# Kernel optimization log

Measured on AMD Instinct MI355X. Metric: run time of the kernel, lower is better.

The kernel has to match this reference:

```python
import jax, jax.numpy as jnp
import numpy as np

WS = 7
SHIFT = 3
NH = 16
DIM = 512
MLP = 2048
EMB = 512
EPS = 1e-6


def _rel_pos_index(ws):
    coords = np.stack(np.meshgrid(np.arange(ws), np.arange(ws), indexing='ij'))  # [2,ws,ws]
    flat = coords.reshape(2, -1)
    rel = flat[:, :, None] - flat[:, None, :]          # [2,N,N]
    rel = rel.transpose(1, 2, 0).copy()                # [N,N,2]
    rel[..., 0] += ws - 1
    rel[..., 1] += ws - 1
    rel[..., 0] *= 2 * ws - 1
    return rel.sum(-1)                                 # [N,N] int


def _shift_mask(H, W, ws, shift):
    img = np.zeros((H, W))
    cnt = 0
    for hs in (slice(0, -ws), slice(-ws, -shift), slice(-shift, None)):
        for wsl in (slice(0, -ws), slice(-ws, -shift), slice(-shift, None)):
            img[hs, wsl] = cnt
            cnt += 1
    win = img.reshape(H // ws, ws, W // ws, ws).transpose(0, 2, 1, 3).reshape(-1, ws * ws)
    diff = win[:, None, :] - win[:, :, None]           # [nW,N,N]
    return np.where(diff != 0, -100.0, 0.0).astype(np.float32)


def setup_inputs() -> dict:
    key = jax.random.key(0)
    ks = jax.random.split(key, 16)
    B, H, W = 16, 56, 56
    C, mlp, emb_dim = DIM, MLP, EMB
    std = 0.02
    inp = {
        'x': jax.random.normal(ks[0], (B, H * W, C), jnp.float32),
        'emb': jax.random.normal(ks[1], (B, emb_dim), jnp.float32),
        'adaLN_w': jax.random.normal(ks[2], (emb_dim, 6 * C), jnp.float32) * std,
        'adaLN_b': jnp.zeros((6 * C,), jnp.float32),
        'qkv_w': jax.random.normal(ks[3], (C, 3 * C), jnp.float32) * std,
        'qkv_b': jnp.zeros((3 * C,), jnp.float32),
        'proj_w': jax.random.normal(ks[4], (C, C), jnp.float32) * std,
        'proj_b': jnp.zeros((C,), jnp.float32),
        'rel_bias_table': jax.random.normal(ks[5], ((2 * WS - 1) ** 2, NH), jnp.float32) * std,
        'ff_w1': jax.random.normal(ks[6], (C, mlp), jnp.float32) * std,
        'ff_b1': jnp.zeros((mlp,), jnp.float32),
        'ff_w2': jax.random.normal(ks[7], (mlp, C), jnp.float32) * std,
        'ff_b2': jnp.zeros((C,), jnp.float32),
        'H': H,
        'W': W,
    }
    return inp


def _ln(t):
    mu = t.mean(-1, keepdims=True)
    var = ((t - mu) ** 2).mean(-1, keepdims=True)
    return (t - mu) / jnp.sqrt(var + EPS)


def reference(x, emb, adaLN_w, adaLN_b, qkv_w, qkv_b, proj_w, proj_b,
              rel_bias_table, ff_w1, ff_b1, ff_w2, ff_b2, H, W):
    B, L, C = x.shape
    dh = C // NH
    scale = dh ** (-0.5)
    N = WS * WS
    nWh, nWw = H // WS, W // WS
    nW = nWh * nWw

    # AdaLN modulation
    mod = jax.nn.silu(emb) @ adaLN_w + adaLN_b
    sh_sa, sc_sa, g_sa, sh_ff, sc_ff, g_ff = jnp.split(mod, 6, axis=-1)

    h = _ln(x) * (1.0 + sc_sa[:, None, :]) + sh_sa[:, None, :]
    h = h.reshape(B, H, W, C)
    h = jnp.roll(h, (-SHIFT, -SHIFT), axis=(1, 2))

    # window partition -> [B*nW, N, C]
    win = h.reshape(B, nWh, WS, nWw, WS, C).transpose(0, 1, 3, 2, 4, 5).reshape(B * nW, N, C)

    qkv = (win @ qkv_w + qkv_b).reshape(B * nW, N, 3, NH, dh).transpose(2, 0, 3, 1, 4)
    q, k, v = qkv[0], qkv[1], qkv[2]                   # [B_, NH, N, dh]
    attn = jnp.einsum('bhnd,bhmd->bhnm', q, k) * scale

    idx = _rel_pos_index(WS)
    bias = rel_bias_table[idx.reshape(-1)].reshape(N, N, NH).transpose(2, 0, 1)
    attn = attn + bias[None]

    mask = jnp.asarray(_shift_mask(H, W, WS, SHIFT))   # [nW,N,N]
    attn = attn.reshape(B, nW, NH, N, N) + mask[None, :, None]
    attn = jax.nn.softmax(attn.reshape(B * nW, NH, N, N), axis=-1)

    out = jnp.einsum('bhnm,bhmd->bnhd', attn, v).reshape(B * nW, N, C)
    out = out @ proj_w + proj_b

    # window reverse + unshift
    h = out.reshape(B, nWh, nWw, WS, WS, C).transpose(0, 1, 3, 2, 4, 5).reshape(B, H, W, C)
    h = jnp.roll(h, (SHIFT, SHIFT), axis=(1, 2)).reshape(B, L, C)

    x = x + g_sa[:, None, :] * h

    h = _ln(x) * (1.0 + sc_ff[:, None, :]) + sh_ff[:, None, :]
    ffo = jax.nn.gelu(h @ ff_w1 + ff_b1, approximate=False) @ ff_w2 + ff_b2
    return x + g_ff[:, None, :] * ffo
```

## Files before the change

kernel.cpp:

```cpp
#include <hip/hip_runtime.h>
#include <cmath>

typedef unsigned short u16;
typedef unsigned short u16x2 __attribute__((ext_vector_type(2)));
typedef unsigned short u16x4 __attribute__((ext_vector_type(4)));
typedef unsigned short u16x8 __attribute__((ext_vector_type(8)));
typedef short s16x8 __attribute__((ext_vector_type(8)));
typedef float f32x4 __attribute__((ext_vector_type(4)));
typedef float f32x2 __attribute__((ext_vector_type(2)));

#define B_SZ 16
#define HW 56
#define L_TOK 3136
#define C_DIM 512
#define NHEAD 16
#define DHEAD 32
#define WS7 7
#define NWIN 49
#define ROWS_TOTAL 50176
#define MLP_DIM 2048

__device__ __forceinline__ float bf2f(u16 u) {
    union { unsigned int i; float f; } z;
    z.i = ((unsigned int)u) << 16;
    return z.f;
}
__device__ __forceinline__ u16 f2bf(float f) {
    union { float f; unsigned int i; } z;
    z.f = f;
    unsigned int r = z.i + 0x7fffu + ((z.i >> 16) & 1u);
    return (u16)(r >> 16);
}

__device__ __forceinline__ void gl_lds16(const u16* g, u16* l) {
    __builtin_amdgcn_global_load_lds(
        (const __attribute__((address_space(1))) unsigned int*)g,
        (__attribute__((address_space(3))) unsigned int*)l,
        16, 0, 0);
}

__global__ __launch_bounds__(256)
void mod_kernel(const float* __restrict__ emb, const float* __restrict__ w,
                const float* __restrict__ bias, float* __restrict__ mod)
{
    int b = blockIdx.y;
    int o = blockIdx.x * 256 + threadIdx.x;
    __shared__ float se[512];
    for (int i = threadIdx.x; i < 512; i += 256) {
        float e = emb[b * 512 + i];
        se[i] = e / (1.0f + expf(-e));
    }
    __syncthreads();
    float acc = bias[o];
    #pragma unroll 8
    for (int k = 0; k < 512; ++k)
        acc += se[k] * w[(size_t)k * 3072 + o];
    mod[b * 3072 + o] = acc;
}

__global__ __launch_bounds__(1024)
void transpose_kernel(const float* __restrict__ W, u16* __restrict__ Wt, int K, int N)
{
    __shared__ float tile[32][33];
    int k0 = blockIdx.x * 32, n0 = blockIdx.y * 32;
    tile[threadIdx.y][threadIdx.x] = W[(size_t)(k0 + threadIdx.y) * N + (n0 + threadIdx.x)];
    __syncthreads();
    Wt[(size_t)(n0 + threadIdx.y) * K + (k0 + threadIdx.x)] = f2bf(tile[threadIdx.x][threadIdx.y]);
}

template<int WINDOWED>
__global__ __launch_bounds__(256)
void ln_kernel(const float* __restrict__ xin, const float* __restrict__ mod,
               u16* __restrict__ out, int shOff, int scOff, int rowBase)
{
    int wv   = threadIdx.x >> 6;
    int lane = threadIdx.x & 63;
    int rbl = blockIdx.x * 4 + wv;
    int rb  = rbl + rowBase;
    int b = rb / L_TOK, l = rb - b * L_TOK;
    const float* xr = xin + (size_t)rb * C_DIM;
    int c0 = lane * 8;
    f32x4 u0 = *(const f32x4*)(xr + c0);
    f32x4 u1 = *(const f32x4*)(xr + c0 + 4);
    float s = u0.x + u0.y + u0.z + u0.w + u1.x + u1.y + u1.z + u1.w;
    float q = u0.x*u0.x + u0.y*u0.y + u0.z*u0.z + u0.w*u0.w
            + u1.x*u1.x + u1.y*u1.y + u1.z*u1.z + u1.w*u1.w;
    #pragma unroll
    for (int off = 32; off > 0; off >>= 1) {
        s += __shfl_xor(s, off);
        q += __shfl_xor(q, off);
    }
    float mu = s * (1.0f / 512.0f);
    float var = q * (1.0f / 512.0f) - mu * mu;
    float rstd = rsqrtf(var + 1e-6f);
    const float* mb = mod + b * 3072;
    f32x4 sc0 = *(const f32x4*)(mb + scOff + c0);
    f32x4 sc1 = *(const f32x4*)(mb + scOff + c0 + 4);
    f32x4 sh0 = *(const f32x4*)(mb + shOff + c0);
    f32x4 sh1 = *(const f32x4*)(mb + shOff + c0 + 4);
    float y[8];
    y[0] = (u0.x - mu) * rstd * (1.0f + sc0.x) + sh0.x;
    y[1] = (u0.y - mu) * rstd * (1.0f + sc0.y) + sh0.y;
    y[2] = (u0.z - mu) * rstd * (1.0f + sc0.z) + sh0.z;
    y[3] = (u0.w - mu) * rstd * (1.0f + sc0.w) + sh0.w;
    y[4] = (u1.x - mu) * rstd * (1.0f + sc1.x) + sh1.x;
    y[5] = (u1.y - mu) * rstd * (1.0f + sc1.y) + sh1.y;
    y[6] = (u1.z - mu) * rstd * (1.0f + sc1.z) + sh1.z;
    y[7] = (u1.w - mu) * rstd * (1.0f + sc1.w) + sh1.w;
    size_t drow;
    if (WINDOWED) {
        int hh = l / HW, ww = l - hh * HW;
        int hs = hh - 3; if (hs < 0) hs += HW;
        int ws2 = ww - 3; if (ws2 < 0) ws2 += HW;
        int wi = (hs / WS7) * 8 + (ws2 / WS7);
        int n  = (hs % WS7) * WS7 + (ws2 % WS7);
        int b_local = rbl / L_TOK;
        drow = (size_t)((b_local * 64 + wi) * NWIN + n);
    } else {
        drow = (size_t)rbl;
    }
    u16x8 o;
    #pragma unroll
    for (int i = 0; i < 8; ++i) o[i] = f2bf(y[i]);
    *(u16x8*)(out + drow * C_DIM + c0) = o;
}

template<int EPI>
__global__ __launch_bounds__(256)
void gemm128(const u16* __restrict__ A, const u16* __restrict__ Bt,
             const float* __restrict__ bias, void* __restrict__ outv,
             const float* __restrict__ resid, const float* __restrict__ mod,
             int N, int K, int rowOffset)
{
    __shared__ u16 sA[3][128][32];
    __shared__ u16 sB[3][128][32];
    const int tid  = threadIdx.x;
    const int lane = tid & 63;
    const int wave = tid >> 6;
    const int wr = (wave >> 1) * 64;
    const int wc = (wave & 1) * 64;
    const int quad = lane >> 4;
    const int mrow = lane & 15;
    const int rowBase = blockIdx.x * 128;
    const int colBase = blockIdx.y * 128;

    const int r0   = wave * 32;
    const int lrow = lane >> 2;
    const int lcol = (lane & 3) * 8;
    const u16* gA = A  + (size_t)(rowBase + r0 + lrow) * K + lcol;
    const u16* gB = Bt + (size_t)(colBase + r0 + lrow) * K + lcol;
    const size_t gstep = (size_t)16 * K;

    f32x4 acc[4][4] = {};
    const int nt = K >> 5;

#define STAGE(bi, kk) do {                                 \
    gl_lds16(gA + (kk),         &sA[bi][r0][0]);           \
    gl_lds16(gA + (kk) + gstep, &sA[bi][r0 + 16][0]);      \
    gl_lds16(gB + (kk),         &sB[bi][r0][0]);           \
    gl_lds16(gB + (kk) + gstep, &sB[bi][r0 + 16][0]);      \
} while (0)

    STAGE(0, 0);
    STAGE(1, 32);
    asm volatile("s_waitcnt vmcnt(4)" ::: "memory");
    __builtin_amdgcn_s_barrier();

    int cur = 0, pre = 2;
    for (int t = 0; t < nt; ++t) {
        if (t + 2 < nt) STAGE(pre, (t + 2) * 32);
        s16x8 af[4], bg[4];
        #pragma unroll
        for (int tt = 0; tt < 4; ++tt) {
            af[tt] = *(const s16x8*)&sA[cur][wr + tt * 16 + mrow][quad * 8];
            bg[tt] = *(const s16x8*)&sB[cur][wc + tt * 16 + mrow][quad * 8];
        }
        #pragma unroll
        for (int tm = 0; tm < 4; ++tm)
            #pragma unroll
            for (int tn = 0; tn < 4; ++tn)
                acc[tm][tn] = __builtin_amdgcn_mfma_f32_16x16x32_bf16(
                    af[tm], bg[tn], acc[tm][tn], 0, 0, 0);
        if (t + 1 < nt) {
            if (t + 2 < nt)
                asm volatile("s_waitcnt vmcnt(4) lgkmcnt(0)" ::: "memory");
            else
                asm volatile("s_waitcnt vmcnt(0) lgkmcnt(0)" ::: "memory");
            __builtin_amdgcn_s_barrier();
        }
        cur = (cur == 2) ? 0 : cur + 1;
        pre = (pre == 2) ? 0 : pre + 1;
    }
#undef STAGE

    #pragma unroll
    for (int tm = 0; tm < 4; ++tm) {
        #pragma unroll
        for (int tn = 0; tn < 4; ++tn) {
            int col = colBase + wc + tn * 16 + mrow;
            float bv = bias[col];
            #pragma unroll
            for (int i = 0; i < 4; ++i) {
                int r = rowBase + wr + tm * 16 + quad * 4 + i;
                float v = acc[tm][tn][i] + bv;
                if constexpr (EPI == 0) {
                    ((u16*)outv)[(size_t)r * N + col] = f2bf(v);
                } else if constexpr (EPI == 1) {
                    float g = 0.5f * v * (1.0f + erff(v * 0.70710678118654752f));
                    ((u16*)outv)[(size_t)r * N + col] = f2bf(g);
                } else if constexpr (EPI == 2) {
                    int rg = r + rowOffset;
                    int b = rg / L_TOK;
                    int rem = rg - b * L_TOK;
                    int wi = rem / NWIN;
                    int n  = rem - wi * NWIN;
                    int hs  = (wi >> 3) * WS7 + n / WS7;
                    int ws2 = (wi & 7) * WS7 + n % WS7;
                    int hh = hs + 3;  if (hh >= HW)  hh -= HW;
                    int ww = ws2 + 3; if (ww >= HW)  ww -= HW;
                    size_t dst = ((size_t)(b * L_TOK + hh * HW + ww)) * C_DIM + col;
                    float g = mod[b * 3072 + 1024 + col];
                    ((float*)outv)[dst] = resid[dst] + g * v;
                } else {
                    int rg = r + rowOffset;
                    int b = rg / L_TOK;
                    size_t dst = (size_t)rg * C_DIM + col;
                    float g = mod[b * 3072 + 2560 + col];
                    ((float*)outv)[dst] = resid[dst] + g * v;
                }
            }
        }
    }
}

__global__ __launch_bounds__(256)
void attn_mfma(const u16* __restrict__ qkv, const float* __restrict__ bias_table,
               u16* __restrict__ out)
{
    const int w    = blockIdx.x;
    const int hg   = blockIdx.y;
    const int wave = threadIdx.x >> 6;
    const int lane = threadIdx.x & 63;
    const int h    = hg * 4 + wave;
    const int wi   = w & 63;
    const int quad = lane >> 4;
    const int mrow = lane & 15;

    __shared__ u16 sP[4][64][72];
    __shared__ u16 sVt[4][32][72];
    __shared__ float sBias[4][169];

    const u16* qb = qkv + (size_t)w * NWIN * 1536 + h * DHEAD;

    for (int e = lane; e < 169; e += 64)
        sBias[wave][e] = bias_table[e * NHEAD + h];

    #pragma unroll
    for (int rr = 0; rr < 4; ++rr) {
        int e = rr * 64 + lane;
        int r = e >> 2, d0 = (e & 3) * 8;
        u16x8 vv = {};
        if (e < 196)
            vv = *(const u16x8*)(qb + (size_t)r * 1536 + 1024 + d0);
        #pragma unroll
        for (int j = 0; j < 8; ++j)
            sVt[wave][d0 + j][r] = vv[j];
    }

    s16x8 qf[4], kf[4];
    #pragma unroll
    for (int t = 0; t < 4; ++t) {
        int r = t * 16 + mrow; if (r > 48) r = 48;
        qf[t] = *(const s16x8*)(qb + (size_t)r * 1536 + quad * 8);
        kf[t] = *(const s16x8*)(qb + (size_t)r * 1536 + 512 + quad * 8);
    }
    __syncthreads();

    f32x4 sacc[4][4] = {};
    #pragma unroll
    for (int tm = 0; tm < 4; ++tm)
        #pragma unroll
        for (int tn = 0; tn < 4; ++tn)
            sacc[tm][tn] = __builtin_amdgcn_mfma_f32_16x16x32_bf16(
                qf[tm], kf[tn], sacc[tm][tn], 0, 0, 0);

    const float scale = 0.17677669529663687f;
    const int wh = wi >> 3, ww = wi & 7;

    int khA[4], kwA[4], rkA[4], nOK[4];
    #pragma unroll
    for (int tn = 0; tn < 4; ++tn) {
        int n = tn * 16 + mrow;
        nOK[tn] = (n < NWIN);
        int nc = n > 48 ? 48 : n;
        khA[tn] = nc / 7; kwA[tn] = nc - khA[tn] * 7;
        int gkh = wh * 7 + khA[tn], gkw = ww * 7 + kwA[tn];
        rkA[tn] = (gkh < 49 ? 0 : (gkh < 53 ? 1 : 2)) * 3
                + (gkw < 49 ? 0 : (gkw < 53 ? 1 : 2));
    }

    #pragma unroll
    for (int tm = 0; tm < 4; ++tm) {
        #pragma unroll
        for (int i = 0; i < 4; ++i) {
            int m = tm * 16 + quad * 4 + i;
            int mc = m > 48 ? 48 : m;
            int qh = mc / 7, qw = mc - qh * 7;
            int gqh = wh * 7 + qh, gqw = ww * 7 + qw;
            int rq = (gqh < 49 ? 0 : (gqh < 53 ? 1 : 2)) * 3
                   + (gqw < 49 ? 0 : (gqw < 53 ? 1 : 2));
            float v[4];
            #pragma unroll
            for (int tn = 0; tn < 4; ++tn) {
                float s = sacc[tm][tn][i] * scale;
                s += sBias[wave][(qh - khA[tn] + 6) * 13 + (qw - kwA[tn] + 6)];
                if (rq != rkA[tn]) s -= 100.0f;
                v[tn] = nOK[tn] ? s : -1e30f;
            }
            float mx = fmaxf(fmaxf(v[0], v[1]), fmaxf(v[2], v[3]));
            mx = fmaxf(mx, __shfl_xor(mx, 1));
            mx = fmaxf(mx, __shfl_xor(mx, 2));
            mx = fmaxf(mx, __shfl_xor(mx, 4));
            mx = fmaxf(mx, __shfl_xor(mx, 8));
            float p0 = __expf(v[0] - mx), p1 = __expf(v[1] - mx);
            float p2 = __expf(v[2] - mx), p3 = __expf(v[3] - mx);
            float sum = p0 + p1 + p2 + p3;
            sum += __shfl_xor(sum, 1);
            sum += __shfl_xor(sum, 2);
            sum += __shfl_xor(sum, 4);
            sum += __shfl_xor(sum, 8);
            float inv = 1.0f / sum;
            float pp[4] = { p0 * inv, p1 * inv, p2 * inv, p3 * inv };
            #pragma unroll
            for (int tn = 0; tn < 4; ++tn) {
                float po = __shfl_xor(pp[tn], 1);
                if (!(mrow & 1)) {
                    unsigned int pk = (unsigned int)f2bf(pp[tn])
                                    | ((unsigned int)f2bf(po) << 16);
                    *(unsigned int*)&sP[wave][m][tn * 16 + mrow] = pk;
                }
            }
        }
    }
    __syncthreads();

    f32x4 oacc[2][4] = {};
    #pragma unroll
    for (int ks = 0; ks < 2; ++ks) {
        s16x8 vf[2], pf[4];
        #pragma unroll
        for (int td = 0; td < 2; ++td)
            vf[td] = *(const s16x8*)&sVt[wave][td * 16 + mrow][ks * 32 + quad * 8];
        #pragma unroll
        for (int tm = 0; tm < 4; ++tm)
            pf[tm] = *(const s16x8*)&sP[wave][tm * 16 + mrow][ks * 32 + quad * 8];
        #pragma unroll
        for (int td = 0; td < 2; ++td)
            #pragma unroll
            for (int tm = 0; tm < 4; ++tm)
                oacc[td][tm] = __builtin_amdgcn_mfma_f32_16x16x32_bf16(
                    vf[td], pf[tm], oacc[td][tm], 0, 0, 0);
    }

    #pragma unroll
    for (int tm = 0; tm < 4; ++tm) {
        int m = tm * 16 + mrow;
        if (m < NWIN) {
            u16* orow = out + ((size_t)(w * NWIN + m)) * C_DIM + h * DHEAD;
            #pragma unroll
            for (int td = 0; td < 2; ++td) {
                u16x4 ov;
                #pragma unroll
                for (int i = 0; i < 4; ++i) ov[i] = f2bf(oacc[td][tm][i]);
                *(u16x4*)(orow + td * 16 + quad * 4) = ov;
            }
        }
    }
}

extern "C" void kernel_launch(void* const* d_in, const int* in_sizes, int n_in,
                              void* d_out, int out_size, void* d_ws, size_t ws_size,
                              hipStream_t stream)
{
    const float* x       = (const float*)d_in[0];
    const float* emb     = (const float*)d_in[1];
    const float* adaLN_w = (const float*)d_in[2];
    const float* adaLN_b = (const float*)d_in[3];
    const float* qkv_w   = (const float*)d_in[4];
    const float* qkv_b   = (const float*)d_in[5];
    const float* proj_w  = (const float*)d_in[6];
    const float* proj_b  = (const float*)d_in[7];
    const float* relb    = (const float*)d_in[8];
    const float* ff_w1   = (const float*)d_in[9];
    const float* ff_b1   = (const float*)d_in[10];
    const float* ff_w2   = (const float*)d_in[11];
    const float* ff_b2   = (const float*)d_in[12];
    float* outp = (float*)d_out;

    char* ws = (char*)d_ws;
    float* mod   = (float*)(ws + 0);
    u16* wT_qkv  = (u16*)(ws + 196608);
    u16* wT_proj = (u16*)(ws + 1769472);
    u16* wT_ff1  = (u16*)(ws + 2293760);
    u16* wT_ff2  = (u16*)(ws + 4390912);
    char* slots  = ws + 6488064;

    const size_t perB_S = (size_t)L_TOK * C_DIM * sizeof(u16);
    const size_t perB_L = (size_t)L_TOK * MLP_DIM * sizeof(u16);

    int CB = 4;
    if (ws_size >= 6488064 + 8 * (perB_S + perB_L)) CB = 8;

    const int nChunks   = B_SZ / CB;
    const int chunkRows = CB * L_TOK;
    u16* slotS = (u16*)slots;
    u16* slotL = (u16*)(slots + (size_t)CB * perB_S);

    mod_kernel<<<dim3(12, 16), dim3(256), 0, stream>>>(emb, adaLN_w, adaLN_b, mod);
    transpose_kernel<<<dim3(16, 48), dim3(32, 32), 0, stream>>>(qkv_w,  wT_qkv, 512, 1536);
    transpose_kernel<<<dim3(16, 16), dim3(32, 32), 0, stream>>>(proj_w, wT_proj, 512, 512);
    transpose_kernel<<<dim3(16, 64), dim3(32, 32), 0, stream>>>(ff_w1,  wT_ff1, 512, 2048);
    transpose_kernel<<<dim3(64, 16), dim3(32, 32), 0, stream>>>(ff_w2,  wT_ff2, 2048, 512);

    for (int c = 0; c < nChunks; ++c) {
        int row0 = c * chunkRows;
        ln_kernel<1><<<dim3(chunkRows / 4), dim3(256), 0, stream>>>(
            x, mod, slotS, 0, 512, row0);
        gemm128<0><<<dim3(chunkRows / 128, 12), dim3(256), 0, stream>>>(
            slotS, wT_qkv, qkv_b, slotL, nullptr, mod, 1536, 512, 0);
        attn_mfma<<<dim3(CB * 64, 4), dim3(256), 0, stream>>>(slotL, relb, slotS);
        gemm128<2><<<dim3(chunkRows / 128, 4), dim3(256), 0, stream>>>(
            slotS, wT_proj, proj_b, outp, x, mod, 512, 512, row0);
        ln_kernel<0><<<dim3(chunkRows / 4), dim3(256), 0, stream>>>(
            outp, mod, slotS, 1536, 2048, row0);
        gemm128<1><<<dim3(chunkRows / 128, 16), dim3(256), 0, stream>>>(
            slotS, wT_ff1, ff_b1, slotL, nullptr, mod, 2048, 512, 0);
        gemm128<3><<<dim3(chunkRows / 128, 4), dim3(256), 0, stream>>>(
            slotL, wT_ff2, ff_b2, outp, outp, mod, 512, 2048, row0);
    }
}
```

Baseline: 1.159 ms.

## Remap GEMM workgroups across XCDs, double-buffer LDS, and allow full-batch chunks

The GEMM grid becomes 1D, and block IDs are remapped so consecutive logical tiles land on the same XCD. Row-major tile order within each XCD should improve L2 reuse of A rows and weight tiles. The LDS pipeline drops from triple to double buffering with a full vmcnt(0) wait each step, which saves shared memory but exposes more global load latency. The host can also use a 16-image chunk when the workspace is large enough, cutting the number of kernel launches.

```diff
diff --git a/kernel.cpp b/kernel.cpp
--- a/kernel.cpp
+++ b/kernel.cpp
@@ -130,10 +130,10 @@
 void gemm128(const u16* __restrict__ A, const u16* __restrict__ Bt,
              const float* __restrict__ bias, void* __restrict__ outv,
              const float* __restrict__ resid, const float* __restrict__ mod,
-             int N, int K, int rowOffset)
-{
-    __shared__ u16 sA[3][128][32];
-    __shared__ u16 sB[3][128][32];
+             int N, int K, int rowOffset, int nyb)
+{
+    __shared__ u16 sA[2][128][32];
+    __shared__ u16 sB[2][128][32];
     const int tid  = threadIdx.x;
     const int lane = tid & 63;
     const int wave = tid >> 6;
@@ -141,8 +141,17 @@
     const int wc = (wave & 1) * 64;
     const int quad = lane >> 4;
     const int mrow = lane & 15;
-    const int rowBase = blockIdx.x * 128;
-    const int colBase = blockIdx.y * 128;
+
+    const int nwg  = gridDim.x;
+    const int orig = blockIdx.x;
+    const int xq = nwg >> 3, xr = nwg & 7;
+    const int xcd = orig & 7, xidx = orig >> 3;
+    const int wgid = (xcd < xr ? xcd * (xq + 1)
+                               : xr * (xq + 1) + (xcd - xr) * xq) + xidx;
+    const int bx = wgid / nyb;
+    const int by = wgid - bx * nyb;
+    const int rowBase = bx * 128;
+    const int colBase = by * 128;
 
     const int r0   = wave * 32;
     const int lrow = lane >> 2;
@@ -162,13 +171,12 @@
 } while (0)
 
     STAGE(0, 0);
-    STAGE(1, 32);
-    asm volatile("s_waitcnt vmcnt(4)" ::: "memory");
+    asm volatile("s_waitcnt vmcnt(0)" ::: "memory");
     __builtin_amdgcn_s_barrier();
 
-    int cur = 0, pre = 2;
     for (int t = 0; t < nt; ++t) {
-        if (t + 2 < nt) STAGE(pre, (t + 2) * 32);
+        const int cur = t & 1;
+        if (t + 1 < nt) STAGE(cur ^ 1, (t + 1) << 5);
         s16x8 af[4], bg[4];
         #pragma unroll
         for (int tt = 0; tt < 4; ++tt) {
@@ -182,14 +190,9 @@
                 acc[tm][tn] = __builtin_amdgcn_mfma_f32_16x16x32_bf16(
                     af[tm], bg[tn], acc[tm][tn], 0, 0, 0);
         if (t + 1 < nt) {
-            if (t + 2 < nt)
-                asm volatile("s_waitcnt vmcnt(4) lgkmcnt(0)" ::: "memory");
-            else
-                asm volatile("s_waitcnt vmcnt(0) lgkmcnt(0)" ::: "memory");
+            asm volatile("s_waitcnt vmcnt(0) lgkmcnt(0)" ::: "memory");
             __builtin_amdgcn_s_barrier();
         }
-        cur = (cur == 2) ? 0 : cur + 1;
-        pre = (pre == 2) ? 0 : pre + 1;
     }
 #undef STAGE
 
@@ -409,10 +412,12 @@
     const size_t perB_L = (size_t)L_TOK * MLP_DIM * sizeof(u16);
 
     int CB = 4;
-    if (ws_size >= 6488064 + 8 * (perB_S + perB_L)) CB = 8;
+    if (ws_size >= 6488064 + 8  * (perB_S + perB_L)) CB = 8;
+    if (ws_size >= 6488064 + 16 * (perB_S + perB_L)) CB = 16;
 
     const int nChunks   = B_SZ / CB;
     const int chunkRows = CB * L_TOK;
+    const int nrb       = chunkRows / 128;
     u16* slotS = (u16*)slots;
     u16* slotL = (u16*)(slots + (size_t)CB * perB_S);
 
@@ -426,16 +431,16 @@
         int row0 = c * chunkRows;
         ln_kernel<1><<<dim3(chunkRows / 4), dim3(256), 0, stream>>>(
             x, mod, slotS, 0, 512, row0);
-        gemm128<0><<<dim3(chunkRows / 128, 12), dim3(256), 0, stream>>>(
-            slotS, wT_qkv, qkv_b, slotL, nullptr, mod, 1536, 512, 0);
+        gemm128<0><<<dim3(nrb * 12), dim3(256), 0, stream>>>(
+            slotS, wT_qkv, qkv_b, slotL, nullptr, mod, 1536, 512, 0, 12);
         attn_mfma<<<dim3(CB * 64, 4), dim3(256), 0, stream>>>(slotL, relb, slotS);
-        gemm128<2><<<dim3(chunkRows / 128, 4), dim3(256), 0, stream>>>(
-            slotS, wT_proj, proj_b, outp, x, mod, 512, 512, row0);
+        gemm128<2><<<dim3(nrb * 4), dim3(256), 0, stream>>>(
+            slotS, wT_proj, proj_b, outp, x, mod, 512, 512, row0, 4);
         ln_kernel<0><<<dim3(chunkRows / 4), dim3(256), 0, stream>>>(
             outp, mod, slotS, 1536, 2048, row0);
-        gemm128<1><<<dim3(chunkRows / 128, 16), dim3(256), 0, stream>>>(
-            slotS, wT_ff1, ff_b1, slotL, nullptr, mod, 2048, 512, 0);
-        gemm128<3><<<dim3(chunkRows / 128, 4), dim3(256), 0, stream>>>(
-            slotL, wT_ff2, ff_b2, outp, outp, mod, 512, 2048, row0);
-    }
-}
+        gemm128<1><<<dim3(nrb * 16), dim3(256), 0, stream>>>(
+            slotS, wT_ff1, ff_b1, slotL, nullptr, mod, 2048, 512, 0, 16);
+        gemm128<3><<<dim3(nrb * 4), dim3(256), 0, stream>>>(
+            slotL, wT_ff2, ff_b2, outp, outp, mod, 512, 2048, row0, 4);
+    }
+}
```

Result: faster. 1.072 ms (-7.5%).
